# Kernel tuning notes

Measured on AMD Instinct MI355X. Metric: run time of the kernel, lower is better.

The kernel has to match this reference:

```python
import jax, jax.numpy as jnp
import numpy as np
import math

B, MSA, L, D = 1, 64, 256, 512
H = 8
DH = D // H  # 64


def setup_inputs() -> dict:
    key = jax.random.key(0)
    ks = jax.random.split(key, 6)
    x = jax.random.normal(ks[0], (B, MSA, L, D), dtype=jnp.float32)
    Wq = jax.random.normal(ks[1], (D, D), dtype=jnp.float32) * (1.0 / math.sqrt(D))
    Wk = jax.random.normal(ks[2], (D, D), dtype=jnp.float32) * (1.0 / math.sqrt(D))
    Wv = jax.random.normal(ks[3], (D, D), dtype=jnp.float32) * (1.0 / math.sqrt(D))
    aK = jax.random.normal(ks[4], (L, L, DH), dtype=jnp.float32)
    aV = jax.random.normal(ks[5], (L, L, DH), dtype=jnp.float32)
    return {"x": x, "Wq": Wq, "Wk": Wk, "Wv": Wv, "aK": aK, "aV": aV}


def _proj(t, W, b, m, l, h, dh):
    # nn.Linear(bias=False): t @ W.T, then split heads -> (B,H,MSA,L,dh)
    y = jnp.einsum('bmld,ed->bmle', t, W).reshape(b, m, l, h, dh)
    return jnp.transpose(y, (0, 3, 1, 2, 4))


def reference(x, Wq, Wk, Wv, aK, aV):
    b, m, l, d = x.shape
    h, dh = H, DH
    q = _proj(x, Wq, b, m, l, h, dh)  # (B,H,MSA,L,dh)
    k = _proj(x, Wk, b, m, l, h, dh)
    v = _proj(x, Wv, b, m, l, h, dh)
    # content score + relative-position score
    e1 = jnp.einsum('bhmid,bhmjd->bhmij', q, k)           # (B,H,MSA,L,L)
    e2 = jnp.einsum('bhmid,ijd->bhmij', q, aK)            # (B,H,MSA,L,L)
    alpha = jax.nn.softmax((e1 + e2) / math.sqrt(dh), axis=-1)
    z1 = jnp.einsum('bhmij,bhmjd->bhmid', alpha, v)       # content output
    z2 = jnp.einsum('bhmij,ijd->bhmid', alpha, aV)        # relative-V output
    z = (z1 + z2).sum(axis=2)                             # sum over MSA -> (B,H,L,dh)
    out = jnp.transpose(z, (0, 2, 1, 3)).reshape(b, l, d) # (B,L,D)
    return out
```

## Files before the change

kernel.cpp:

```cpp
#include <hip/hip_runtime.h>

#define THREADS 256

typedef unsigned short u16;
typedef __attribute__((ext_vector_type(8))) short bf16x8;
typedef __attribute__((ext_vector_type(4))) float f32x4;

__device__ __forceinline__ u16 f2bf(float f) {
  unsigned int u = __float_as_uint(f);
  u += 0x7fffu + ((u >> 16) & 1u);
  return (u16)(u >> 16);
}
__device__ __forceinline__ float bf2f(u16 s) {
  return __uint_as_float(((unsigned int)s) << 16);
}
__device__ __forceinline__ bf16x8 ld8g(const u16* p) {
  return *reinterpret_cast<const bf16x8*>(p);
}
__device__ __forceinline__ bf16x8 ld8s(const u16* p) {
  return *reinterpret_cast<const bf16x8*>(p);
}
__device__ __forceinline__ void st4bf(u16* dst, float4 v) {
  unsigned int lo = (unsigned int)f2bf(v.x) | ((unsigned int)f2bf(v.y) << 16);
  unsigned int hi = (unsigned int)f2bf(v.z) | ((unsigned int)f2bf(v.w) << 16);
  uint2 u; u.x = lo; u.y = hi;
  *reinterpret_cast<uint2*>(dst) = u;
}
__device__ __forceinline__ uint4 pack8(float4 a, float4 b) {
  uint4 r;
  r.x = (unsigned int)f2bf(a.x) | ((unsigned int)f2bf(a.y) << 16);
  r.y = (unsigned int)f2bf(a.z) | ((unsigned int)f2bf(a.w) << 16);
  r.z = (unsigned int)f2bf(b.x) | ((unsigned int)f2bf(b.y) << 16);
  r.w = (unsigned int)f2bf(b.z) | ((unsigned int)f2bf(b.w) << 16);
  return r;
}
typedef __attribute__((address_space(1))) const unsigned int g_u32;
typedef __attribute__((address_space(3))) unsigned int l_u32;
__device__ __forceinline__ void async16(const u16* g, u16* l) {
  __builtin_amdgcn_global_load_lds((g_u32*)g, (l_u32*)l, 16, 0, 0);
}

__global__ __launch_bounds__(THREADS) void cast_xw(
    const float* __restrict__ x, const float* __restrict__ wq,
    const float* __restrict__ wk, const float* __restrict__ wv,
    u16* __restrict__ xb, u16* __restrict__ wqb, u16* __restrict__ wkb,
    u16* __restrict__ wvb) {
  int t = blockIdx.x * THREADS + threadIdx.x;
  if (t < 2097152) {
    st4bf(xb + t * 4, reinterpret_cast<const float4*>(x)[t]);
  } else if (t < 2162688) {
    int q = t - 2097152;
    st4bf(wqb + q * 4, reinterpret_cast<const float4*>(wq)[q]);
  } else if (t < 2228224) {
    int q = t - 2162688;
    st4bf(wkb + q * 4, reinterpret_cast<const float4*>(wk)[q]);
  } else if (t < 2293760) {
    int q = t - 2228224;
    st4bf(wvb + q * 4, reinterpret_cast<const float4*>(wv)[q]);
  }
}

__global__ __launch_bounds__(THREADS) void proj_gemm(
    const u16* __restrict__ xb, const u16* __restrict__ wb,
    u16* __restrict__ qh, u16* __restrict__ kb, u16* __restrict__ vt) {
  const int bid = blockIdx.x;
  const int swzb = (bid & 7) * 192 + (bid >> 3);
  const int bm = swzb / 12, bn = swzb % 12;
  const int tid = threadIdx.x;
  const int wave = tid >> 6, lane = tid & 63;
  const int quad = lane >> 4, l15 = lane & 15;
  __shared__ __align__(16) u16 smem[9216];
  u16* At = smem;
  u16* Bt = smem + 4096;

  const int rowL = lane >> 2;
  const int chunkL = (lane & 3) ^ ((lane >> 3) & 3);
  const u16* gA = xb + (size_t)(bm * 128 + wave * 32 + rowL) * 512 + chunkL * 8;
  const u16* gB = wb + (size_t)(bn * 128 + wave * 32 + rowL) * 512 + chunkL * 8;
  u16* lA = At + wave * 1024;
  u16* lB = Bt + wave * 1024;

  const int rw0 = (wave & 1) * 64, cw0 = (wave >> 1) * 64;
  const int swz = (quad ^ ((l15 >> 1) & 3)) * 8;

  f32x4 acc[4][4];
#pragma unroll
  for (int mt = 0; mt < 4; ++mt)
#pragma unroll
    for (int nt = 0; nt < 4; ++nt) acc[mt][nt] = (f32x4){0.f, 0.f, 0.f, 0.f};

  for (int s = 0; s < 16; ++s) {
    __syncthreads();
    async16(gA + s * 32, lA);
    async16(gA + s * 32 + 8192, lA + 512);
    async16(gB + s * 32, lB);
    async16(gB + s * 32 + 8192, lB + 512);
    __syncthreads();
    bf16x8 af[4], bf[4];
#pragma unroll
    for (int mt = 0; mt < 4; ++mt)
      af[mt] = ld8s(At + (rw0 + mt * 16 + l15) * 32 + swz);
#pragma unroll
    for (int nt = 0; nt < 4; ++nt)
      bf[nt] = ld8s(Bt + (cw0 + nt * 16 + l15) * 32 + swz);
#pragma unroll
    for (int mt = 0; mt < 4; ++mt)
#pragma unroll
      for (int nt = 0; nt < 4; ++nt)
        acc[mt][nt] = __builtin_amdgcn_mfma_f32_16x16x32_bf16(af[mt], bf[nt], acc[mt][nt], 0, 0, 0);
  }

  const int mat = bn >> 2;
  const int h0 = (bn & 3) * 2;
  const int m = bm >> 1;
  const int l0 = (bm & 1) * 128;

  if (mat < 2) {
    u16* dstb = (mat == 0) ? qh : kb;
    const int il = tid >> 1, cc = (tid & 1) * 32;
#pragma unroll
    for (int p = 0; p < 2; ++p) {
      __syncthreads();
      if ((wave >> 1) == p) {
#pragma unroll
        for (int mt = 0; mt < 4; ++mt)
#pragma unroll
          for (int nt = 0; nt < 4; ++nt)
#pragma unroll
            for (int r = 0; r < 4; ++r)
              smem[(rw0 + mt * 16 + quad * 4 + r) * 72 + nt * 16 + l15] =
                  f2bf(acc[mt][nt][r]);
      }
      __syncthreads();
      u16* dst = dstb + ((size_t)((h0 + p) * 64 + m) * 256 + l0 + il) * 64 + cc;
      uint4 v0 = *reinterpret_cast<uint4*>(&smem[il * 72 + cc]);
      uint4 v1 = *reinterpret_cast<uint4*>(&smem[il * 72 + cc + 8]);
      uint4 v2 = *reinterpret_cast<uint4*>(&smem[il * 72 + cc + 16]);
      uint4 v3 = *reinterpret_cast<uint4*>(&smem[il * 72 + cc + 24]);
      *reinterpret_cast<uint4*>(dst) = v0;
      *reinterpret_cast<uint4*>(dst + 8) = v1;
      *reinterpret_cast<uint4*>(dst + 16) = v2;
      *reinterpret_cast<uint4*>(dst + 24) = v3;
    }
  } else {
    const int tl = tid >> 2, cc = (tid & 3) * 32;
#pragma unroll
    for (int p = 0; p < 2; ++p) {
      __syncthreads();
      if ((wave >> 1) == p) {
#pragma unroll
        for (int mt = 0; mt < 4; ++mt)
#pragma unroll
          for (int nt = 0; nt < 4; ++nt)
#pragma unroll
            for (int r = 0; r < 4; ++r)
              smem[(nt * 16 + l15) * 136 + rw0 + mt * 16 + quad * 4 + r] =
                  f2bf(acc[mt][nt][r]);
      }
      __syncthreads();
      int hm = (h0 + p) * 64 + m;
      u16* dst = vt + (size_t)hm * 16384 + tl * 256 + l0 + cc;
      uint4 v0 = *reinterpret_cast<uint4*>(&smem[tl * 136 + cc]);
      uint4 v1 = *reinterpret_cast<uint4*>(&smem[tl * 136 + cc + 8]);
      uint4 v2 = *reinterpret_cast<uint4*>(&smem[tl * 136 + cc + 16]);
      uint4 v3 = *reinterpret_cast<uint4*>(&smem[tl * 136 + cc + 24]);
      *reinterpret_cast<uint4*>(dst) = v0;
      *reinterpret_cast<uint4*>(dst + 8) = v1;
      *reinterpret_cast<uint4*>(dst + 16) = v2;
      *reinterpret_cast<uint4*>(dst + 24) = v3;
    }
  }
}

__global__ __launch_bounds__(THREADS) void e2_k(
    const u16* __restrict__ qh, const float* __restrict__ aK,
    u16* __restrict__ e2g) {
  const int hmt = blockIdx.x >> 8, i = blockIdx.x & 255;
  const int tid = threadIdx.x;
  const int wave = tid >> 6, lane = tid & 63;
  const int quad = lane >> 4, l15 = lane & 15;
  __shared__ u16 aKl[256 * 72];
  __shared__ u16 qL[64 * 72];
#pragma unroll
  for (int c = 0; c < 8; ++c) {
    int fidx = c * 2048 + tid * 8;
    int j = fidx >> 6, d = fidx & 63;
    float4 f0 = *reinterpret_cast<const float4*>(aK + i * 16384 + fidx);
    float4 f1 = *reinterpret_cast<const float4*>(aK + i * 16384 + fidx + 4);
    *reinterpret_cast<uint4*>(&aKl[j * 72 + d]) = pack8(f0, f1);
  }
#pragma unroll
  for (int c = 0; c < 4; ++c) {
    int r = c * 16 + (tid >> 4);
    int dd = (tid & 15) * 4;
    uint2 v = *reinterpret_cast<const uint2*>(
        qh + ((size_t)(hmt * 64 + r) * 256 + i) * 64 + dd);
    *reinterpret_cast<uint2*>(&qL[r * 72 + dd]) = v;
  }
  __syncthreads();
  f32x4 acc[16];
#pragma unroll
  for (int nt = 0; nt < 16; ++nt) acc[nt] = (f32x4){0.f, 0.f, 0.f, 0.f};
  bf16x8 a[2];
#pragma unroll
  for (int ks = 0; ks < 2; ++ks)
    a[ks] = ld8s(&qL[(wave * 16 + l15) * 72 + ks * 32 + quad * 8]);
#pragma unroll
  for (int nt = 0; nt < 16; ++nt) {
#pragma unroll
    for (int ks = 0; ks < 2; ++ks) {
      bf16x8 b = ld8s(&aKl[(nt * 16 + l15) * 72 + ks * 32 + quad * 8]);
      acc[nt] = __builtin_amdgcn_mfma_f32_16x16x32_bf16(a[ks], b, acc[nt], 0, 0, 0);
    }
  }
  __syncthreads();
  u16* S = aKl;
#pragma unroll
  for (int nt = 0; nt < 16; ++nt)
#pragma unroll
    for (int r = 0; r < 4; ++r)
      S[(wave * 16 + quad * 4 + r) * 264 + nt * 16 + l15] = f2bf(acc[nt][r]);
  __syncthreads();
#pragma unroll
  for (int c = 0; c < 8; ++c) {
    int lin = c * 2048 + tid * 8;
    int row = lin >> 8, col = lin & 255;
    uint4 v = *reinterpret_cast<uint4*>(&S[row * 264 + col]);
    *reinterpret_cast<uint4*>(e2g + ((size_t)(hmt * 64 + row) * 256 + i) * 256 + col) = v;
  }
}

__global__ __launch_bounds__(THREADS, 2) void attn_f(
    const u16* __restrict__ qh, const u16* __restrict__ kb,
    const u16* __restrict__ vt, const u16* __restrict__ e2g,
    u16* __restrict__ betap, u16* __restrict__ z1q) {
  const int bi = blockIdx.x;
  const int it = bi >> 7;
  const int hmc = bi & 127;
  const int h = hmc >> 4, mc = hmc & 15;
  const int tid = threadIdx.x;
  const int wave = tid >> 6, lane = tid & 63;
  const int quad = lane >> 4, l15 = lane & 15;
  __shared__ u16 As[4 * 4224];
  u16* W = &As[wave * 4224];
  const int i0 = it * 64 + wave * 16;

  f32x4 betaacc[16];
  f32x4 acc2[4];
#pragma unroll
  for (int nt = 0; nt < 16; ++nt) betaacc[nt] = (f32x4){0.f, 0.f, 0.f, 0.f};
#pragma unroll
  for (int nt = 0; nt < 4; ++nt) acc2[nt] = (f32x4){0.f, 0.f, 0.f, 0.f};

  for (int mi = 0; mi < 4; ++mi) {
    const int hm = h * 64 + mc * 4 + mi;
    f32x4 acc[16];
    const u16* e2p = e2g + ((size_t)hm * 256 + i0 + quad * 4) * 256 + l15;
#pragma unroll
    for (int nt = 0; nt < 16; ++nt)
#pragma unroll
      for (int r = 0; r < 4; ++r)
        acc[nt][r] = bf2f(e2p[r * 256 + nt * 16]);
    bf16x8 a[2];
#pragma unroll
    for (int ks = 0; ks < 2; ++ks)
      a[ks] = ld8g(qh + ((size_t)hm * 256 + i0 + l15) * 64 + ks * 32 + quad * 8);
#pragma unroll
    for (int nt = 0; nt < 16; ++nt) {
#pragma unroll
      for (int ks = 0; ks < 2; ++ks) {
        bf16x8 b = ld8g(kb + ((size_t)hm * 256 + nt * 16 + l15) * 64 + ks * 32 + quad * 8);
        acc[nt] = __builtin_amdgcn_mfma_f32_16x16x32_bf16(a[ks], b, acc[nt], 0, 0, 0);
      }
    }
#pragma unroll
    for (int r = 0; r < 4; ++r) {
      float mx = -3.0e38f;
#pragma unroll
      for (int nt = 0; nt < 16; ++nt) mx = fmaxf(mx, acc[nt][r]);
      for (int msk = 1; msk < 16; msk <<= 1) mx = fmaxf(mx, __shfl_xor(mx, msk));
      float s = 0.f;
#pragma unroll
      for (int nt = 0; nt < 16; ++nt) {
        float p = __expf((acc[nt][r] - mx) * 0.125f);
        acc[nt][r] = p;
        s += p;
      }
      for (int msk = 1; msk < 16; msk <<= 1) s += __shfl_xor(s, msk);
      float inv = 1.0f / s;
      int lrow = quad * 4 + r;
#pragma unroll
      for (int nt = 0; nt < 16; ++nt) {
        float av = acc[nt][r] * inv;
        betaacc[nt][r] += av;
        W[lrow * 264 + nt * 16 + l15] = f2bf(av);
      }
    }
#pragma unroll
    for (int ks = 0; ks < 8; ++ks) {
      bf16x8 a2 = ld8s(&W[l15 * 264 + ks * 32 + quad * 8]);
#pragma unroll
      for (int nt = 0; nt < 4; ++nt) {
        bf16x8 b2 = ld8g(vt + (size_t)hm * 16384 + (nt * 16 + l15) * 256 + ks * 32 + quad * 8);
        acc2[nt] = __builtin_amdgcn_mfma_f32_16x16x32_bf16(a2, b2, acc2[nt], 0, 0, 0);
      }
    }
  }

#pragma unroll
  for (int nt = 0; nt < 16; ++nt)
#pragma unroll
    for (int r = 0; r < 4; ++r)
      W[(quad * 4 + r) * 264 + nt * 16 + l15] = f2bf(betaacc[nt][r]);
#pragma unroll
  for (int c = 0; c < 8; ++c) {
    int lin = c * 512 + lane * 8;
    int row = lin >> 8, col = lin & 255;
    uint4 v = *reinterpret_cast<uint4*>(&W[row * 264 + col]);
    *reinterpret_cast<uint4*>(
        betap + ((size_t)hmc * 256 + it * 64 + wave * 16 + row) * 256 + col) = v;
  }
#pragma unroll
  for (int nt = 0; nt < 4; ++nt)
#pragma unroll
    for (int r = 0; r < 4; ++r)
      W[(quad * 4 + r) * 72 + nt * 16 + l15] = f2bf(acc2[nt][r]);
  {
    int row = lane >> 2, col = (lane & 3) * 16;
    uint4 v0 = *reinterpret_cast<uint4*>(&W[row * 72 + col]);
    uint4 v1 = *reinterpret_cast<uint4*>(&W[row * 72 + col + 8]);
    u16* dst = z1q + ((size_t)hmc * 256 + it * 64 + wave * 16 + row) * 64 + col;
    *reinterpret_cast<uint4*>(dst) = v0;
    *reinterpret_cast<uint4*>(dst + 8) = v1;
  }
}

__global__ __launch_bounds__(THREADS) void z2f_k(
    const u16* __restrict__ betap, const u16* __restrict__ z1q,
    const float* __restrict__ aV, float* __restrict__ out) {
  const int i = blockIdx.x;
  const int tid = threadIdx.x;
  const int wave = tid >> 6, lane = tid & 63;
  const int quad = lane >> 4, l15 = lane & 15;
  __shared__ u16 aVl[64 * 264];
  __shared__ float bj[8 * 256];
  __shared__ float z2L[512];
#pragma unroll
  for (int c = 0; c < 8; ++c) {
    int fidx = c * 2048 + tid * 8;
    int j = fidx >> 6, d = fidx & 63;
    float4 f0 = *reinterpret_cast<const float4*>(aV + (size_t)i * 16384 + fidx);
    float4 f1 = *reinterpret_cast<const float4*>(aV + (size_t)i * 16384 + fidx + 4);
    float fv[8] = {f0.x, f0.y, f0.z, f0.w, f1.x, f1.y, f1.z, f1.w};
#pragma unroll
    for (int u = 0; u < 8; ++u) aVl[(d + u) * 264 + j] = f2bf(fv[u]);
  }
  {
    int h = tid >> 5, j0 = (tid & 31) * 8;
    const u16* src = betap + (size_t)(h * 16) * 65536 + i * 256 + j0;
    float s[8] = {0.f, 0.f, 0.f, 0.f, 0.f, 0.f, 0.f, 0.f};
#pragma unroll
    for (int m = 0; m < 16; ++m) {
      uint4 v = *reinterpret_cast<const uint4*>(src + (size_t)m * 65536);
      const u16* pv = reinterpret_cast<const u16*>(&v);
#pragma unroll
      for (int u = 0; u < 8; ++u) s[u] += bf2f(pv[u]);
    }
#pragma unroll
    for (int u = 0; u < 8; ++u) bj[h * 256 + j0 + u] = s[u];
  }
  __syncthreads();
  f32x4 acc = (f32x4){0.f, 0.f, 0.f, 0.f};
#pragma unroll
  for (int ks = 0; ks < 8; ++ks) {
    u16 ab[8];
    if (l15 < 8) {
      const float* bp = &bj[l15 * 256 + ks * 32 + quad * 8];
#pragma unroll
      for (int u = 0; u < 8; ++u) ab[u] = f2bf(bp[u]);
    } else {
#pragma unroll
      for (int u = 0; u < 8; ++u) ab[u] = 0;
    }
    bf16x8 a = *reinterpret_cast<bf16x8*>(ab);
    bf16x8 b = ld8s(&aVl[(wave * 16 + l15) * 264 + ks * 32 + quad * 8]);
    acc = __builtin_amdgcn_mfma_f32_16x16x32_bf16(a, b, acc, 0, 0, 0);
  }
#pragma unroll
  for (int r = 0; r < 4; ++r) {
    int hh = quad * 4 + r;
    if (hh < 8) z2L[hh * 64 + wave * 16 + l15] = acc[r];
  }
  __syncthreads();
#pragma unroll
  for (int c = 0; c < 2; ++c) {
    int e = c * 256 + tid;
    int h = e >> 6, d = e & 63;
    float s = z2L[e];
    const u16* base = z1q + ((size_t)(h * 16) * 256 + i) * 64 + d;
#pragma unroll
    for (int m = 0; m < 16; ++m) s += bf2f(base[(size_t)m * 16384]);
    out[(size_t)i * 512 + e] = s;
  }
}

extern "C" void kernel_launch(void* const* d_in, const int* in_sizes, int n_in,
                              void* d_out, int out_size, void* d_ws, size_t ws_size,
                              hipStream_t stream) {
  const float* x  = (const float*)d_in[0];
  const float* wq = (const float*)d_in[1];
  const float* wk = (const float*)d_in[2];
  const float* wv = (const float*)d_in[3];
  const float* aK = (const float*)d_in[4];
  const float* aV = (const float*)d_in[5];
  float* out = (float*)d_out;

  char* ws = (char*)d_ws;
  u16* xb    = (u16*)(ws + 0);
  u16* wqb   = (u16*)(ws + 16777216);
  u16* wkb   = (u16*)(ws + 17301504);
  u16* wvb   = (u16*)(ws + 17825792);
  u16* betap = (u16*)(ws + 18350080);
  u16* qh    = (u16*)(ws + 35127296);
  u16* kb    = (u16*)(ws + 51904512);
  u16* vt    = (u16*)(ws + 68681728);
  u16* e2g   = (u16*)(ws + 85458944);
  u16* z1q   = xb;

  cast_xw<<<8960, THREADS, 0, stream>>>(x, wq, wk, wv, xb, wqb, wkb, wvb);
  proj_gemm<<<1536, THREADS, 0, stream>>>(xb, wqb, qh, kb, vt);
  e2_k<<<2048, THREADS, 0, stream>>>(qh, aK, e2g);
  attn_f<<<512, THREADS, 0, stream>>>(qh, kb, vt, e2g, betap, z1q);
  z2f_k<<<256, THREADS, 0, stream>>>(betap, z1q, aV, out);
}
```

Measured before the change: 261.3 us.

## Split attention key dimension across wave pairs and drop softmax max subtraction

Each attention block now covers 32 query rows instead of 64. Two waves share each 16-row group, with each wave handling half of the 256 keys. Row sums are combined through shared memory and the partial z1 outputs are summed before writing. This doubles the grid to 1024 blocks and halves per-wave accumulator registers, which allows three blocks per CU. The softmax max-subtraction and its shuffle reduction are removed to save work, which risks exp overflow if scores grow large.

```diff
diff --git a/kernel.cpp b/kernel.cpp
--- a/kernel.cpp
+++ b/kernel.cpp
@@ -230,34 +230,37 @@
   }
 }
 
-__global__ __launch_bounds__(THREADS, 2) void attn_f(
+__global__ __launch_bounds__(THREADS, 3) void attn_f(
     const u16* __restrict__ qh, const u16* __restrict__ kb,
     const u16* __restrict__ vt, const u16* __restrict__ e2g,
     u16* __restrict__ betap, u16* __restrict__ z1q) {
   const int bi = blockIdx.x;
-  const int it = bi >> 7;
+  const int it2 = bi >> 7;
   const int hmc = bi & 127;
   const int h = hmc >> 4, mc = hmc & 15;
   const int tid = threadIdx.x;
   const int wave = tid >> 6, lane = tid & 63;
+  const int ig = wave >> 1, jh = wave & 1;
   const int quad = lane >> 4, l15 = lane & 15;
-  __shared__ u16 As[4 * 4224];
-  u16* W = &As[wave * 4224];
-  const int i0 = it * 64 + wave * 16;
-
-  f32x4 betaacc[16];
+  __shared__ __align__(16) u16 As[2 * 16 * 264];
+  __shared__ float sums[2][2][2][16];
+  u16* Wg = &As[ig * 16 * 264];
+  const int i0 = it2 * 32 + ig * 16;
+  const int jb = jh * 128;
+
+  f32x4 betaacc[8];
   f32x4 acc2[4];
 #pragma unroll
-  for (int nt = 0; nt < 16; ++nt) betaacc[nt] = (f32x4){0.f, 0.f, 0.f, 0.f};
+  for (int nt = 0; nt < 8; ++nt) betaacc[nt] = (f32x4){0.f, 0.f, 0.f, 0.f};
 #pragma unroll
   for (int nt = 0; nt < 4; ++nt) acc2[nt] = (f32x4){0.f, 0.f, 0.f, 0.f};
 
   for (int mi = 0; mi < 4; ++mi) {
     const int hm = h * 64 + mc * 4 + mi;
-    f32x4 acc[16];
-    const u16* e2p = e2g + ((size_t)hm * 256 + i0 + quad * 4) * 256 + l15;
-#pragma unroll
-    for (int nt = 0; nt < 16; ++nt)
+    f32x4 acc[8];
+    const u16* e2p = e2g + ((size_t)hm * 256 + i0 + quad * 4) * 256 + jb + l15;
+#pragma unroll
+    for (int nt = 0; nt < 8; ++nt)
 #pragma unroll
       for (int r = 0; r < 4; ++r)
         acc[nt][r] = bf2f(e2p[r * 256 + nt * 16]);
@@ -266,72 +269,86 @@
     for (int ks = 0; ks < 2; ++ks)
       a[ks] = ld8g(qh + ((size_t)hm * 256 + i0 + l15) * 64 + ks * 32 + quad * 8);
 #pragma unroll
-    for (int nt = 0; nt < 16; ++nt) {
+    for (int nt = 0; nt < 8; ++nt) {
 #pragma unroll
       for (int ks = 0; ks < 2; ++ks) {
-        bf16x8 b = ld8g(kb + ((size_t)hm * 256 + nt * 16 + l15) * 64 + ks * 32 + quad * 8);
+        bf16x8 b = ld8g(kb + ((size_t)hm * 256 + jb + nt * 16 + l15) * 64 + ks * 32 + quad * 8);
         acc[nt] = __builtin_amdgcn_mfma_f32_16x16x32_bf16(a[ks], b, acc[nt], 0, 0, 0);
       }
     }
+    float ps[4];
 #pragma unroll
     for (int r = 0; r < 4; ++r) {
-      float mx = -3.0e38f;
-#pragma unroll
-      for (int nt = 0; nt < 16; ++nt) mx = fmaxf(mx, acc[nt][r]);
-      for (int msk = 1; msk < 16; msk <<= 1) mx = fmaxf(mx, __shfl_xor(mx, msk));
       float s = 0.f;
 #pragma unroll
-      for (int nt = 0; nt < 16; ++nt) {
-        float p = __expf((acc[nt][r] - mx) * 0.125f);
+      for (int nt = 0; nt < 8; ++nt) {
+        float p = __expf(acc[nt][r] * 0.125f);
         acc[nt][r] = p;
         s += p;
       }
       for (int msk = 1; msk < 16; msk <<= 1) s += __shfl_xor(s, msk);
-      float inv = 1.0f / s;
-      int lrow = quad * 4 + r;
-#pragma unroll
-      for (int nt = 0; nt < 16; ++nt) {
+      ps[r] = s;
+    }
+    if (l15 == 0) {
+#pragma unroll
+      for (int r = 0; r < 4; ++r) sums[mi & 1][ig][jh][quad * 4 + r] = ps[r];
+    }
+    __syncthreads();
+#pragma unroll
+    for (int r = 0; r < 4; ++r) {
+      int row = quad * 4 + r;
+      float inv = 1.0f / (sums[mi & 1][ig][0][row] + sums[mi & 1][ig][1][row]);
+#pragma unroll
+      for (int nt = 0; nt < 8; ++nt) {
         float av = acc[nt][r] * inv;
         betaacc[nt][r] += av;
-        W[lrow * 264 + nt * 16 + l15] = f2bf(av);
-      }
-    }
-#pragma unroll
-    for (int ks = 0; ks < 8; ++ks) {
-      bf16x8 a2 = ld8s(&W[l15 * 264 + ks * 32 + quad * 8]);
+        Wg[row * 264 + jb + nt * 16 + l15] = f2bf(av);
+      }
+    }
+#pragma unroll
+    for (int ks = 0; ks < 4; ++ks) {
+      bf16x8 a2 = ld8s(&Wg[l15 * 264 + jb + ks * 32 + quad * 8]);
 #pragma unroll
       for (int nt = 0; nt < 4; ++nt) {
-        bf16x8 b2 = ld8g(vt + (size_t)hm * 16384 + (nt * 16 + l15) * 256 + ks * 32 + quad * 8);
+        bf16x8 b2 = ld8g(vt + (size_t)hm * 16384 + (nt * 16 + l15) * 256 + jb + ks * 32 + quad * 8);
         acc2[nt] = __builtin_amdgcn_mfma_f32_16x16x32_bf16(a2, b2, acc2[nt], 0, 0, 0);
       }
     }
   }
 
 #pragma unroll
-  for (int nt = 0; nt < 16; ++nt)
+  for (int nt = 0; nt < 8; ++nt)
 #pragma unroll
     for (int r = 0; r < 4; ++r)
-      W[(quad * 4 + r) * 264 + nt * 16 + l15] = f2bf(betaacc[nt][r]);
-#pragma unroll
-  for (int c = 0; c < 8; ++c) {
-    int lin = c * 512 + lane * 8;
+      Wg[(quad * 4 + r) * 264 + jb + nt * 16 + l15] = f2bf(betaacc[nt][r]);
+  __syncthreads();
+#pragma unroll
+  for (int c = 0; c < 4; ++c) {
+    int lin = c * 2048 + tid * 8;
     int row = lin >> 8, col = lin & 255;
-    uint4 v = *reinterpret_cast<uint4*>(&W[row * 264 + col]);
+    uint4 v = *reinterpret_cast<uint4*>(&As[row * 264 + col]);
     *reinterpret_cast<uint4*>(
-        betap + ((size_t)hmc * 256 + it * 64 + wave * 16 + row) * 256 + col) = v;
-  }
+        betap + ((size_t)hmc * 256 + it2 * 32 + row) * 256 + col) = v;
+  }
+  __syncthreads();
+  float* zl = reinterpret_cast<float*>(As);
 #pragma unroll
   for (int nt = 0; nt < 4; ++nt)
 #pragma unroll
     for (int r = 0; r < 4; ++r)
-      W[(quad * 4 + r) * 72 + nt * 16 + l15] = f2bf(acc2[nt][r]);
+      zl[((jh * 2 + ig) * 16 + quad * 4 + r) * 64 + nt * 16 + l15] = acc2[nt][r];
+  __syncthreads();
   {
-    int row = lane >> 2, col = (lane & 3) * 16;
-    uint4 v0 = *reinterpret_cast<uint4*>(&W[row * 72 + col]);
-    uint4 v1 = *reinterpret_cast<uint4*>(&W[row * 72 + col + 8]);
-    u16* dst = z1q + ((size_t)hmc * 256 + it * 64 + wave * 16 + row) * 64 + col;
-    *reinterpret_cast<uint4*>(dst) = v0;
-    *reinterpret_cast<uint4*>(dst + 8) = v1;
+    int rl = wave * 8 + (lane >> 3);
+    int ig2 = rl >> 4, r2 = rl & 15, d0 = (lane & 7) * 8;
+    u16 ob[8];
+#pragma unroll
+    for (int u = 0; u < 8; ++u)
+      ob[u] = f2bf(zl[((0 * 2 + ig2) * 16 + r2) * 64 + d0 + u] +
+                   zl[((1 * 2 + ig2) * 16 + r2) * 64 + d0 + u]);
+    *reinterpret_cast<uint4*>(
+        z1q + ((size_t)hmc * 256 + it2 * 32 + rl) * 64 + d0) =
+        *reinterpret_cast<uint4*>(ob);
   }
 }
 
@@ -430,6 +447,6 @@
   cast_xw<<<8960, THREADS, 0, stream>>>(x, wq, wk, wv, xb, wqb, wkb, wvb);
   proj_gemm<<<1536, THREADS, 0, stream>>>(xb, wqb, qh, kb, vt);
   e2_k<<<2048, THREADS, 0, stream>>>(qh, aK, e2g);
-  attn_f<<<512, THREADS, 0, stream>>>(qh, kb, vt, e2g, betap, z1q);
+  attn_f<<<1024, THREADS, 0, stream>>>(qh, kb, vt, e2g, betap, z1q);
   z2f_k<<<256, THREADS, 0, stream>>>(betap, z1q, aV, out);
 }
```

Measured after the change: 289.3 us. +10.7%, slower.
